# Optimization experiments

Hardware: AMD Instinct MI355X
Metric: run time of the kernel (lower is better)

## Reference

```python
import jax, jax.numpy as jnp
import numpy as np

BS, N, C = 16, 4096, 32
HID, OUT = 16, 1
N_ORBS = 64


def _linear_init(key, fan_in, fan_out):
    # torch nn.Linear default: U(-1/sqrt(fan_in), 1/sqrt(fan_in)) for W and b
    kw, kb = jax.random.split(key)
    bound = 1.0 / np.sqrt(fan_in)
    W = jax.random.uniform(kw, (fan_in, fan_out), minval=-bound, maxval=bound, dtype=jnp.float32)
    b = jax.random.uniform(kb, (fan_out,), minval=-bound, maxval=bound, dtype=jnp.float32)
    return W, b


def setup_inputs() -> dict:
    key = jax.random.key(0)
    ks = jax.random.split(key, 8)
    coords = jax.random.normal(ks[0], (BS, N, 2, 2), dtype=jnp.float32)
    # orbit identifiers live at coords[:, :, 1, 1]; draw from a fixed discrete set
    orb_ids = jax.random.randint(ks[1], (BS, N), 0, N_ORBS).astype(jnp.float32)
    # guarantee all N_ORBS values appear so unique() has exactly N_ORBS entries
    orb_ids = orb_ids.at[0, :N_ORBS].set(jnp.arange(N_ORBS, dtype=jnp.float32))
    coords = coords.at[:, :, 1, 1].set(orb_ids)
    vals = jax.random.normal(ks[2], (BS, N, C), dtype=jnp.float32)
    mask = jax.random.bernoulli(ks[3], 0.9, (BS, N))
    W1, b1 = _linear_init(ks[4], C, HID)
    W2, b2 = _linear_init(ks[5], HID, HID)
    W3, b3 = _linear_init(ks[6], HID, OUT)
    return {"coords": coords, "vals": vals, "mask": mask,
            "W1": W1, "b1": b1, "W2": W2, "b2": b2, "W3": W3, "b3": b3,
            "n_orbs": N_ORBS}


def reference(coords, vals, mask, W1, b1, W2, b2, W3, b3, n_orbs):
    orb = coords[:, :, 1, 1]                              # (bs, n)
    # torch.unique over the whole tensor -> sorted global unique orbit values
    uniq = jnp.unique(orb, size=n_orbs)                   # (n_orbs,)
    # orbit-membership mask; einsum contraction over n == masked broadcast + sum(dim=1)
    orbs_mask = (orb[:, :, None] == uniq[None, None, :]).astype(vals.dtype)  # (bs, n, n_orbs)
    masked_vals = jnp.where(mask[..., None], vals, jnp.zeros((), vals.dtype))  # (bs, n, c)
    agg_orbs = jnp.einsum('bnk,bnc->bkc', orbs_mask, masked_vals)              # (bs, n_orbs, c)
    empty_orbs = agg_orbs.sum(axis=-1) == 0               # (bs, n_orbs)
    h = jax.nn.relu(agg_orbs @ W1 + b1)
    h = jax.nn.relu(h @ W2 + b2)
    transf = h @ W3 + b3                                  # (bs, n_orbs, out_dim)
    transf = jnp.where(empty_orbs[..., None], jnp.zeros((), transf.dtype), transf)
    return transf.sum(axis=1)                             # (bs, out_dim)
```

## Files before the change

### kernel.cpp

```cpp
#include <hip/hip_runtime.h>

#define BS     16
#define NPTS   4096
#define CH     32
#define HID    16
#define NORB   64
#define SLICES 32
#define PPB    (NPTS / SLICES)

__global__ __launch_bounds__(256) void gigp_agg(
    const float* __restrict__ coords,
    const float* __restrict__ vals,
    const int*   __restrict__ mask,
    float*       __restrict__ ws)
{
    __shared__ float agg[NORB][CH + 1];

    const int tid   = threadIdx.x;
    const int b     = blockIdx.x >> 5;
    const int slice = blockIdx.x & (SLICES - 1);

    for (int i = tid; i < NORB * (CH + 1); i += 256)
        (&agg[0][0])[i] = 0.0f;
    __syncthreads();

    const int c4 = tid & 7;
    const int pl = tid >> 3;
    const float4* vals4 = (const float4*)vals;

    #pragma unroll
    for (int it = 0; it < PPB / 32; ++it) {
        const int n  = slice * PPB + it * 32 + pl;
        const int gi = b * NPTS + n;
        const int   k = (int)coords[(size_t)gi * 4 + 3];
        const int   m = mask[gi];
        const float4 v = vals4[(size_t)gi * 8 + c4];
        if (m) {
            atomicAdd(&agg[k][c4 * 4 + 0], v.x);
            atomicAdd(&agg[k][c4 * 4 + 1], v.y);
            atomicAdd(&agg[k][c4 * 4 + 2], v.z);
            atomicAdd(&agg[k][c4 * 4 + 3], v.w);
        }
    }
    __syncthreads();

    for (int e = tid; e < NORB * CH; e += 256) {
        const int k = e >> 5;
        const int c = e & 31;
        const float v = agg[k][c];
        if (v != 0.0f)
            atomicAdd(&ws[((size_t)b * NORB + k) * CH + c], v);
    }
}

__global__ __launch_bounds__(64) void gigp_mlp(
    const float* __restrict__ ws,
    const float* __restrict__ W1, const float* __restrict__ b1,
    const float* __restrict__ W2, const float* __restrict__ b2,
    const float* __restrict__ W3, const float* __restrict__ b3,
    float*       __restrict__ out)
{
    const int b = blockIdx.x;
    const int k = threadIdx.x;

    float a[CH];
    const float4* w4 = (const float4*)(ws + ((size_t)b * NORB + k) * CH);
    float chsum = 0.0f;
    #pragma unroll
    for (int i = 0; i < CH / 4; ++i) {
        const float4 t = w4[i];
        a[i * 4 + 0] = t.x; a[i * 4 + 1] = t.y;
        a[i * 4 + 2] = t.z; a[i * 4 + 3] = t.w;
        chsum += t.x + t.y + t.z + t.w;
    }

    float h1[HID];
    #pragma unroll
    for (int j = 0; j < HID; ++j) h1[j] = b1[j];
    #pragma unroll
    for (int cc = 0; cc < CH; ++cc) {
        const float x = a[cc];
        #pragma unroll
        for (int j = 0; j < HID; ++j)
            h1[j] += x * W1[cc * HID + j];
    }
    #pragma unroll
    for (int j = 0; j < HID; ++j) h1[j] = h1[j] > 0.0f ? h1[j] : 0.0f;

    float h2[HID];
    #pragma unroll
    for (int j = 0; j < HID; ++j) h2[j] = b2[j];
    #pragma unroll
    for (int i = 0; i < HID; ++i) {
        const float x = h1[i];
        #pragma unroll
        for (int j = 0; j < HID; ++j)
            h2[j] += x * W2[i * HID + j];
    }
    float o = b3[0];
    #pragma unroll
    for (int i = 0; i < HID; ++i) {
        const float x = h2[i] > 0.0f ? h2[i] : 0.0f;
        o += x * W3[i];
    }
    o = (chsum == 0.0f) ? 0.0f : o;

    #pragma unroll
    for (int off = 32; off > 0; off >>= 1)
        o += __shfl_down(o, off);
    if (k == 0) out[b] = o;
}

extern "C" void kernel_launch(void* const* d_in, const int* in_sizes, int n_in,
                              void* d_out, int out_size, void* d_ws, size_t ws_size,
                              hipStream_t stream) {
    const float* coords = (const float*)d_in[0];
    const float* vals   = (const float*)d_in[1];
    const int*   mask   = (const int*)d_in[2];
    const float* W1     = (const float*)d_in[3];
    const float* b1     = (const float*)d_in[4];
    const float* W2     = (const float*)d_in[5];
    const float* b2     = (const float*)d_in[6];
    const float* W3     = (const float*)d_in[7];
    const float* b3     = (const float*)d_in[8];
    float* out = (float*)d_out;
    float* ws  = (float*)d_ws;

    hipMemsetAsync(ws, 0, (size_t)BS * NORB * CH * sizeof(float), stream);

    gigp_agg<<<BS * SLICES, 256, 0, stream>>>(coords, vals, mask, ws);
    gigp_mlp<<<BS, 64, 0, stream>>>(ws, W1, b1, W2, b2, W3, b3, out);
}
```

Before: 97.47 us.

## Replace global atomics with per-slice partials reduced in MLP kernel, drop memset

The aggregation kernel now writes each block's full shared-memory partial to its own slice of the workspace with vectorized stores, replacing global atomicAdds into a zeroed buffer. This removes the memset launch and atomic contention. The MLP kernel reduces the 32 slice partials per batch in 256 threads before running the MLP on 64 threads. Global loads are also hoisted into registers before the shared-memory zeroing barrier so they overlap. The cost is a larger workspace and a serial 32-slice reduction on only 16 blocks.

```diff
diff --git a/kernel.cpp b/kernel.cpp
--- a/kernel.cpp
+++ b/kernel.cpp
@@ -7,12 +7,13 @@
 #define NORB   64
 #define SLICES 32
 #define PPB    (NPTS / SLICES)
+#define ITERS  (PPB / 32)
 
 __global__ __launch_bounds__(256) void gigp_agg(
     const float* __restrict__ coords,
     const float* __restrict__ vals,
     const int*   __restrict__ mask,
-    float*       __restrict__ ws)
+    float*       __restrict__ part)
 {
     __shared__ float agg[NORB][CH + 1];
 
@@ -22,93 +23,128 @@
 
     for (int i = tid; i < NORB * (CH + 1); i += 256)
         (&agg[0][0])[i] = 0.0f;
-    __syncthreads();
 
     const int c4 = tid & 7;
     const int pl = tid >> 3;
     const float4* vals4 = (const float4*)vals;
 
+    int    kk[ITERS];
+    int    mm[ITERS];
+    float4 vv[ITERS];
     #pragma unroll
-    for (int it = 0; it < PPB / 32; ++it) {
+    for (int it = 0; it < ITERS; ++it) {
         const int n  = slice * PPB + it * 32 + pl;
         const int gi = b * NPTS + n;
-        const int   k = (int)coords[(size_t)gi * 4 + 3];
-        const int   m = mask[gi];
-        const float4 v = vals4[(size_t)gi * 8 + c4];
-        if (m) {
-            atomicAdd(&agg[k][c4 * 4 + 0], v.x);
-            atomicAdd(&agg[k][c4 * 4 + 1], v.y);
-            atomicAdd(&agg[k][c4 * 4 + 2], v.z);
-            atomicAdd(&agg[k][c4 * 4 + 3], v.w);
+        kk[it] = (int)coords[(size_t)gi * 4 + 3];
+        mm[it] = mask[gi];
+        vv[it] = vals4[(size_t)gi * 8 + c4];
+    }
+    __syncthreads();
+
+    #pragma unroll
+    for (int it = 0; it < ITERS; ++it) {
+        if (mm[it]) {
+            const int k = kk[it];
+            atomicAdd(&agg[k][c4 * 4 + 0], vv[it].x);
+            atomicAdd(&agg[k][c4 * 4 + 1], vv[it].y);
+            atomicAdd(&agg[k][c4 * 4 + 2], vv[it].z);
+            atomicAdd(&agg[k][c4 * 4 + 3], vv[it].w);
         }
     }
     __syncthreads();
 
-    for (int e = tid; e < NORB * CH; e += 256) {
-        const int k = e >> 5;
-        const int c = e & 31;
-        const float v = agg[k][c];
-        if (v != 0.0f)
-            atomicAdd(&ws[((size_t)b * NORB + k) * CH + c], v);
+    float4* dst = (float4*)(part + ((size_t)b * SLICES + slice) * NORB * CH);
+    #pragma unroll
+    for (int j = 0; j < 2; ++j) {
+        const int e  = tid + j * 256;
+        const int k  = e >> 3;
+        const int c4v = e & 7;
+        float4 t;
+        t.x = agg[k][c4v * 4 + 0];
+        t.y = agg[k][c4v * 4 + 1];
+        t.z = agg[k][c4v * 4 + 2];
+        t.w = agg[k][c4v * 4 + 3];
+        dst[e] = t;
     }
 }
 
-__global__ __launch_bounds__(64) void gigp_mlp(
-    const float* __restrict__ ws,
+__global__ __launch_bounds__(256) void gigp_mlp(
+    const float* __restrict__ part,
     const float* __restrict__ W1, const float* __restrict__ b1,
     const float* __restrict__ W2, const float* __restrict__ b2,
     const float* __restrict__ W3, const float* __restrict__ b3,
     float*       __restrict__ out)
 {
-    const int b = blockIdx.x;
-    const int k = threadIdx.x;
+    __shared__ float agg[NORB][CH + 1];
 
-    float a[CH];
-    const float4* w4 = (const float4*)(ws + ((size_t)b * NORB + k) * CH);
-    float chsum = 0.0f;
+    const int b   = blockIdx.x;
+    const int tid = threadIdx.x;
+
+    const float4* src = (const float4*)(part + (size_t)b * SLICES * NORB * CH);
+
+    float4 a0 = make_float4(0.f, 0.f, 0.f, 0.f);
+    float4 a1 = make_float4(0.f, 0.f, 0.f, 0.f);
     #pragma unroll
-    for (int i = 0; i < CH / 4; ++i) {
-        const float4 t = w4[i];
-        a[i * 4 + 0] = t.x; a[i * 4 + 1] = t.y;
-        a[i * 4 + 2] = t.z; a[i * 4 + 3] = t.w;
-        chsum += t.x + t.y + t.z + t.w;
+    for (int s = 0; s < SLICES; ++s) {
+        const float4 t0 = src[(size_t)s * (NORB * CH / 4) + tid];
+        const float4 t1 = src[(size_t)s * (NORB * CH / 4) + tid + 256];
+        a0.x += t0.x; a0.y += t0.y; a0.z += t0.z; a0.w += t0.w;
+        a1.x += t1.x; a1.y += t1.y; a1.z += t1.z; a1.w += t1.w;
     }
+    {
+        const int e0 = tid, e1 = tid + 256;
+        const int k0 = e0 >> 3, c0 = (e0 & 7) * 4;
+        const int k1 = e1 >> 3, c1 = (e1 & 7) * 4;
+        agg[k0][c0 + 0] = a0.x; agg[k0][c0 + 1] = a0.y;
+        agg[k0][c0 + 2] = a0.z; agg[k0][c0 + 3] = a0.w;
+        agg[k1][c1 + 0] = a1.x; agg[k1][c1 + 1] = a1.y;
+        agg[k1][c1 + 2] = a1.z; agg[k1][c1 + 3] = a1.w;
+    }
+    __syncthreads();
 
-    float h1[HID];
-    #pragma unroll
-    for (int j = 0; j < HID; ++j) h1[j] = b1[j];
-    #pragma unroll
-    for (int cc = 0; cc < CH; ++cc) {
-        const float x = a[cc];
+    if (tid < NORB) {
+        const int k = tid;
+
+        float chsum = 0.0f;
         #pragma unroll
-        for (int j = 0; j < HID; ++j)
-            h1[j] += x * W1[cc * HID + j];
+        for (int cc = 0; cc < CH; ++cc) chsum += agg[k][cc];
+
+        float h1[HID];
+        #pragma unroll
+        for (int j = 0; j < HID; ++j) h1[j] = b1[j];
+        #pragma unroll
+        for (int cc = 0; cc < CH; ++cc) {
+            const float x = agg[k][cc];
+            #pragma unroll
+            for (int j = 0; j < HID; ++j)
+                h1[j] += x * W1[cc * HID + j];
+        }
+        #pragma unroll
+        for (int j = 0; j < HID; ++j) h1[j] = h1[j] > 0.0f ? h1[j] : 0.0f;
+
+        float h2[HID];
+        #pragma unroll
+        for (int j = 0; j < HID; ++j) h2[j] = b2[j];
+        #pragma unroll
+        for (int i = 0; i < HID; ++i) {
+            const float x = h1[i];
+            #pragma unroll
+            for (int j = 0; j < HID; ++j)
+                h2[j] += x * W2[i * HID + j];
+        }
+        float o = b3[0];
+        #pragma unroll
+        for (int i = 0; i < HID; ++i) {
+            const float x = h2[i] > 0.0f ? h2[i] : 0.0f;
+            o += x * W3[i];
+        }
+        o = (chsum == 0.0f) ? 0.0f : o;
+
+        #pragma unroll
+        for (int off = 32; off > 0; off >>= 1)
+            o += __shfl_down(o, off);
+        if (k == 0) out[b] = o;
     }
-    #pragma unroll
-    for (int j = 0; j < HID; ++j) h1[j] = h1[j] > 0.0f ? h1[j] : 0.0f;
-
-    float h2[HID];
-    #pragma unroll
-    for (int j = 0; j < HID; ++j) h2[j] = b2[j];
-    #pragma unroll
-    for (int i = 0; i < HID; ++i) {
-        const float x = h1[i];
-        #pragma unroll
-        for (int j = 0; j < HID; ++j)
-            h2[j] += x * W2[i * HID + j];
-    }
-    float o = b3[0];
-    #pragma unroll
-    for (int i = 0; i < HID; ++i) {
-        const float x = h2[i] > 0.0f ? h2[i] : 0.0f;
-        o += x * W3[i];
-    }
-    o = (chsum == 0.0f) ? 0.0f : o;
-
-    #pragma unroll
-    for (int off = 32; off > 0; off >>= 1)
-        o += __shfl_down(o, off);
-    if (k == 0) out[b] = o;
 }
 
 extern "C" void kernel_launch(void* const* d_in, const int* in_sizes, int n_in,
@@ -123,11 +159,9 @@
     const float* b2     = (const float*)d_in[6];
     const float* W3     = (const float*)d_in[7];
     const float* b3     = (const float*)d_in[8];
-    float* out = (float*)d_out;
-    float* ws  = (float*)d_ws;
+    float* out  = (float*)d_out;
+    float* part = (float*)d_ws;
 
-    hipMemsetAsync(ws, 0, (size_t)BS * NORB * CH * sizeof(float), stream);
-
-    gigp_agg<<<BS * SLICES, 256, 0, stream>>>(coords, vals, mask, ws);
-    gigp_mlp<<<BS, 64, 0, stream>>>(ws, W1, b1, W2, b2, W3, b3, out);
+    gigp_agg<<<BS * SLICES, 256, 0, stream>>>(coords, vals, mask, part);
+    gigp_mlp<<<BS, 256, 0, stream>>>(part, W1, b1, W2, b2, W3, b3, out);
 }
```

New measurement: 97.44 us. About the same (-0.0%).
